# Optimization experiments

Measured on AMD Instinct MI355X. Metric: run time of the kernel, lower is better.

The kernel has to match this reference:

```python
import jax, jax.numpy as jnp
import numpy as np

D_MODEL = 1024
D_STATE = 16
D_CONV = 4
EXPAND = 2
D_INNER = D_MODEL * EXPAND


def setup_inputs() -> dict:
    key = jax.random.key(0)
    ks = jax.random.split(key, 8)
    B, L = 2, 2048
    x = jax.random.normal(ks[0], (B, L, D_MODEL), dtype=jnp.float32)
    # in_proj: Linear(d_model -> 2*d_inner), no bias
    W_in = jax.random.normal(ks[1], (D_MODEL, 2 * D_INNER), dtype=jnp.float32) / np.sqrt(D_MODEL)
    # depthwise conv1d: (d_inner, 1, d_conv) + bias
    conv_w = jax.random.normal(ks[2], (D_INNER, 1, D_CONV), dtype=jnp.float32) / np.sqrt(D_CONV)
    conv_b = jax.random.normal(ks[3], (D_INNER,), dtype=jnp.float32) * 0.01
    # x_proj: Linear(d_inner -> 2*d_state + 1), no bias
    W_x = jax.random.normal(ks[4], (D_INNER, 2 * D_STATE + 1), dtype=jnp.float32) / np.sqrt(D_INNER)
    # A_log ~ Uniform(-log(d_state), -1)
    A_log = jax.random.uniform(ks[5], (D_INNER, D_STATE), dtype=jnp.float32,
                               minval=-np.log(D_STATE), maxval=-1.0)
    D_param = jnp.ones((D_INNER,), dtype=jnp.float32)
    W_out = jax.random.normal(ks[6], (D_INNER, D_MODEL), dtype=jnp.float32) / np.sqrt(D_INNER)
    return {"x": x, "W_in": W_in, "conv_w": conv_w, "conv_b": conv_b,
            "W_x": W_x, "A_log": A_log, "D_param": D_param, "W_out": W_out}


def _selective_scan(x, delta, A, Bm, Cm):
    # x:(B,L,D), delta:(B,L), A:(D,N), Bm/Cm:(B,L,N)
    Bsz, L, Dd = x.shape
    N = A.shape[1]
    h0 = jnp.zeros((Bsz, Dd, N), dtype=x.dtype)

    def step(h, inp):
        dt, Bt, Ct, xt = inp  # (B,), wait dt:(B,), Bt:(B,N), Ct:(B,N), xt:(B,D)
        A_bar = jnp.exp(dt[:, None, None] * A)          # (B,D,N)
        dB = (dt[:, None] * Bt)[:, None, :]             # (B,1,N)
        h = A_bar * h + dB * xt[:, :, None]             # (B,D,N)
        y = jnp.einsum('bn,bdn->bd', Ct, h)             # (B,D)
        return h, y

    xs = (jnp.swapaxes(delta, 0, 1), jnp.swapaxes(Bm, 0, 1),
          jnp.swapaxes(Cm, 0, 1), jnp.swapaxes(x, 0, 1))
    _, ys = jax.lax.scan(step, h0, xs)                  # ys: (L,B,D)
    return jnp.swapaxes(ys, 0, 1)


def reference(x, W_in, conv_w, conv_b, W_x, A_log, D_param, W_out):
    B, L, _ = x.shape
    xr = x @ W_in                                       # (B,L,2*Di)
    x_inner, res = jnp.split(xr, 2, axis=-1)
    # causal depthwise conv: left-pad d_conv-1, valid conv == torch slice [:L]
    xc = jnp.swapaxes(x_inner, 1, 2)                    # (B,Di,L)
    xc = jax.lax.conv_general_dilated(
        xc, conv_w, window_strides=(1,), padding=[(D_CONV - 1, 0)],
        dimension_numbers=('NCH', 'OIH', 'NCH'), feature_group_count=D_INNER)
    xc = xc + conv_b[None, :, None]
    xc = jnp.swapaxes(xc, 1, 2)                         # (B,L,Di)
    xc = jax.nn.silu(xc)
    ssm_params = xc @ W_x                               # (B,L,1+2N)
    delta = jax.nn.softplus(ssm_params[..., 0])         # (B,L)
    Bm = ssm_params[..., 1:1 + D_STATE]                 # (B,L,N)
    Cm = ssm_params[..., 1 + D_STATE:]                  # (B,L,N)
    A = -jnp.exp(A_log)                                 # (Di,N)
    y = _selective_scan(xc, delta, A, Bm, Cm)           # (B,L,Di)
    y = y + xc * D_param[None, None, :]
    y = y * jax.nn.silu(res)
    return y @ W_out                                    # (B,L,d_model)
```

## Files before the change

### kernel.cpp

```cpp
#include <hip/hip_runtime.h>

#define L_SEQ 2048
#define NB    2
#define DMOD  1024
#define DIN   2048
#define NST   16
#define NROWS (NB*L_SEQ)
#define CL    32
#define NC    (L_SEQ/CL)

typedef unsigned short u16;
typedef _Float16 half8 __attribute__((ext_vector_type(8)));
typedef float f32x4 __attribute__((ext_vector_type(4)));
typedef short short8 __attribute__((ext_vector_type(8)));

__device__ __forceinline__ float siluf(float v){ return v / (1.f + __expf(-v)); }
__device__ __forceinline__ u16 f2h_bits(float v){ _Float16 h = (_Float16)v; return __builtin_bit_cast(u16, h); }
__device__ __forceinline__ float h2f(u16 v){ return (float)__builtin_bit_cast(_Float16, v); }
__device__ __forceinline__ float fexp2(float x){
#if __has_builtin(__builtin_amdgcn_exp2f)
    return __builtin_amdgcn_exp2f(x);
#else
    return __expf(x * 0.69314718056f);
#endif
}

__global__ __launch_bounds__(256)
void f32_to_f16(const float* __restrict__ in, u16* __restrict__ out, int n4)
{
    int i = blockIdx.x * 256 + threadIdx.x;
    if (i >= n4) return;
    float4 v = ((const float4*)in)[i];
    ushort4 o;
    o.x = f2h_bits(v.x); o.y = f2h_bits(v.y); o.z = f2h_bits(v.z); o.w = f2h_bits(v.w);
    *(ushort4*)&out[(size_t)i * 4] = o;
}

__global__ __launch_bounds__(256)
void transpose_to_f16(const float* __restrict__ in, u16* __restrict__ outT, int R, int C)
{
    __shared__ float s[64][65];
    int r0 = blockIdx.y * 64, c0 = blockIdx.x * 64;
    int tc = threadIdx.x & 63, ty = threadIdx.x >> 6;
    #pragma unroll
    for (int j = 0; j < 16; j++) {
        int r = ty + j * 4;
        s[r][tc] = in[(size_t)(r0 + r) * C + c0 + tc];
    }
    __syncthreads();
    #pragma unroll
    for (int j = 0; j < 16; j++) {
        int nn = ty + j * 4;
        outT[(size_t)(c0 + nn) * R + r0 + tc] = f2h_bits(s[tc][nn]);
    }
}

template<int EPI>
__global__ __launch_bounds__(256)
void gemm_mfma(const u16* __restrict__ A, const u16* __restrict__ Bt,
               void* __restrict__ C0v, void* __restrict__ C1v,
               int M, int N, int K)
{
    __shared__ __align__(16) u16 As[128 * 64];
    __shared__ __align__(16) u16 Bs[128 * 64];
    const int tid  = threadIdx.x;
    const int lane = tid & 63;
    const int wid  = tid >> 6;
    const int wm   = wid >> 1, wn = wid & 1;
    const int bm = blockIdx.y * 128, bn = blockIdx.x * 128;

    const int srow  = tid >> 3;
    const int sunit = tid & 7;
    const u16* Ag = A  + (size_t)bm * K;
    const u16* Bg = Bt + (size_t)bn * K;

    f32x4 acc[4][4];
    #pragma unroll
    for (int i = 0; i < 4; i++)
        #pragma unroll
        for (int j = 0; j < 4; j++)
            acc[i][j] = (f32x4){0.f, 0.f, 0.f, 0.f};

    short8 ra[4], rb[4];
    #pragma unroll
    for (int j = 0; j < 4; j++) {
        int row = j * 32 + srow;
        ra[j] = *(const short8*)&Ag[(size_t)row * K + sunit * 8];
        rb[j] = *(const short8*)&Bg[(size_t)row * K + sunit * 8];
    }

    for (int k0 = 0; k0 < K; k0 += 64) {
        __syncthreads();
        #pragma unroll
        for (int j = 0; j < 4; j++) {
            int row  = j * 32 + srow;
            int slot = sunit ^ (row & 7);
            *(short8*)&As[row * 64 + slot * 8] = ra[j];
            *(short8*)&Bs[row * 64 + slot * 8] = rb[j];
        }
        __syncthreads();
        if (k0 + 64 < K) {
            #pragma unroll
            for (int j = 0; j < 4; j++) {
                int row = j * 32 + srow;
                ra[j] = *(const short8*)&Ag[(size_t)row * K + k0 + 64 + sunit * 8];
                rb[j] = *(const short8*)&Bg[(size_t)row * K + k0 + 64 + sunit * 8];
            }
        }
        #pragma unroll
        for (int kk = 0; kk < 2; kk++) {
            half8 af[4], bf[4];
            #pragma unroll
            for (int mi = 0; mi < 4; mi++) {
                int row  = wm * 64 + mi * 16 + (lane & 15);
                int slot = (kk * 4 + (lane >> 4)) ^ (row & 7);
                af[mi] = *(const half8*)&As[row * 64 + slot * 8];
            }
            #pragma unroll
            for (int ni = 0; ni < 4; ni++) {
                int row  = wn * 64 + ni * 16 + (lane & 15);
                int slot = (kk * 4 + (lane >> 4)) ^ (row & 7);
                bf[ni] = *(const half8*)&Bs[row * 64 + slot * 8];
            }
            #pragma unroll
            for (int mi = 0; mi < 4; mi++)
                #pragma unroll
                for (int ni = 0; ni < 4; ni++)
                    acc[mi][ni] = __builtin_amdgcn_mfma_f32_16x16x32_f16(af[mi], bf[ni], acc[mi][ni], 0, 0, 0);
        }
    }

    const int cr = (lane >> 4) * 4;
    const int cc = lane & 15;
    #pragma unroll
    for (int mi = 0; mi < 4; mi++) {
        #pragma unroll
        for (int ni = 0; ni < 4; ni++) {
            #pragma unroll
            for (int q = 0; q < 4; q++) {
                int row = bm + wm * 64 + mi * 16 + cr + q;
                int col = bn + wn * 64 + ni * 16 + cc;
                float v = acc[mi][ni][q];
                if (EPI == 0) {
                    ((float*)C0v)[(size_t)row * N + col] = v;
                } else {
                    int half = N >> 1;
                    if (col < half) ((u16*)C0v)[(size_t)row * half + col] = f2h_bits(v);
                    else            ((u16*)C1v)[(size_t)row * half + col - half] = f2h_bits(siluf(v));
                }
            }
        }
    }
}

__global__ __launch_bounds__(256)
void conv_silu16(const u16* __restrict__ xin16, const float* __restrict__ cw,
                 const float* __restrict__ cb, u16* __restrict__ xc16)
{
    int idx = blockIdx.x * 256 + threadIdx.x;
    int d8 = idx & 255;
    int t  = (idx >> 8) & (L_SEQ - 1);
    int b  = idx >> 19;
    int d  = d8 << 3;
    const float4* cw4 = (const float4*)cw;
    float4 w[8];
    #pragma unroll
    for (int j = 0; j < 8; j++) w[j] = cw4[d + j];
    float acc[8];
    {
        float4 b0 = *(const float4*)&cb[d];
        float4 b1 = *(const float4*)&cb[d + 4];
        acc[0]=b0.x; acc[1]=b0.y; acc[2]=b0.z; acc[3]=b0.w;
        acc[4]=b1.x; acc[5]=b1.y; acc[6]=b1.z; acc[7]=b1.w;
    }
    #pragma unroll
    for (int k = 0; k < 4; k++) {
        int tt = t + k - 3;
        if (tt >= 0) {
            short8 v = *(const short8*)&xin16[((size_t)(b * L_SEQ + tt)) * DIN + d];
            #pragma unroll
            for (int j = 0; j < 8; j++)
                acc[j] = fmaf(h2f((u16)v[j]), (&w[j].x)[k], acc[j]);
        }
    }
    short8 o;
    #pragma unroll
    for (int j = 0; j < 8; j++) o[j] = (short)f2h_bits(siluf(acc[j]));
    *(short8*)&xc16[(size_t)idx * 8] = o;
}

__global__ __launch_bounds__(256)
void transpose_wx16(const float* __restrict__ Wx, u16* __restrict__ WxT16)
{
    int idx = blockIdx.x * 256 + threadIdx.x;
    int n = idx >> 11, k = idx & 2047;
    float v = (n < 33) ? Wx[k * 33 + n] : 0.f;
    WxT16[idx] = f2h_bits(v);
}

__global__ __launch_bounds__(256)
void gemm2_mfma(const u16* __restrict__ A, const u16* __restrict__ Bt, float* __restrict__ pb)
{
    __shared__ __align__(16) u16 As[64 * 64];
    __shared__ __align__(16) u16 Bs[48 * 64];
    const int tid = threadIdx.x, lane = tid & 63, w = tid >> 6;
    const int bm = blockIdx.x * 64;
    const int kz = blockIdx.y;
    const int arow = tid >> 2;
    const int au   = (tid & 3) << 1;
    f32x4 acc[3];
    acc[0] = acc[1] = acc[2] = (f32x4){0.f, 0.f, 0.f, 0.f};

    for (int it = 0; it < 4; ++it) {
        const int k0 = kz * 256 + it * 64;
        short8 ra0 = *(const short8*)&A[(size_t)(bm + arow) * DIN + k0 + au * 8];
        short8 ra1 = *(const short8*)&A[(size_t)(bm + arow) * DIN + k0 + (au + 1) * 8];
        short8 rb0, rb1;
        if (tid < 192) {
            rb0 = *(const short8*)&Bt[(size_t)arow * DIN + k0 + au * 8];
            rb1 = *(const short8*)&Bt[(size_t)arow * DIN + k0 + (au + 1) * 8];
        }
        __syncthreads();
        {
            int s0 = au ^ (arow & 7), s1 = (au + 1) ^ (arow & 7);
            *(short8*)&As[arow * 64 + s0 * 8] = ra0;
            *(short8*)&As[arow * 64 + s1 * 8] = ra1;
            if (tid < 192) {
                *(short8*)&Bs[arow * 64 + s0 * 8] = rb0;
                *(short8*)&Bs[arow * 64 + s1 * 8] = rb1;
            }
        }
        __syncthreads();
        #pragma unroll
        for (int kk = 0; kk < 2; kk++) {
            int r = w * 16 + (lane & 15);
            int sl = (kk * 4 + (lane >> 4)) ^ (r & 7);
            half8 af = *(const half8*)&As[r * 64 + sl * 8];
            #pragma unroll
            for (int ni = 0; ni < 3; ni++) {
                int br = ni * 16 + (lane & 15);
                int bsl = (kk * 4 + (lane >> 4)) ^ (br & 7);
                half8 bf = *(const half8*)&Bs[br * 64 + bsl * 8];
                acc[ni] = __builtin_amdgcn_mfma_f32_16x16x32_f16(af, bf, acc[ni], 0, 0, 0);
            }
        }
    }
    #pragma unroll
    for (int ni = 0; ni < 3; ni++) {
        #pragma unroll
        for (int q = 0; q < 4; q++) {
            int row = bm + w * 16 + (lane >> 4) * 4 + q;
            int col = ni * 16 + (lane & 15);
            pb[((size_t)kz * NROWS + row) * 48 + col] = acc[ni][q];
        }
    }
}

__global__ __launch_bounds__(256)
void gemm2_reduce(const float* __restrict__ pb, float* __restrict__ delta,
                  float* __restrict__ Bm, float* __restrict__ Cm)
{
    int idx = blockIdx.x * 256 + threadIdx.x;
    int row = idx / 48, col = idx - row * 48;
    float s = 0.f;
    #pragma unroll
    for (int kz = 0; kz < 8; kz++) s += pb[(size_t)kz * NROWS * 48 + idx];
    if (col == 0)       delta[row] = fmaxf(s, 0.f) + log1pf(__expf(-fabsf(s)));
    else if (col < 17)  Bm[row * NST + col - 1]  = s;
    else if (col < 33)  Cm[row * NST + col - 17] = s;
}

__global__ __launch_bounds__(256)
void scan_part1_reg(const u16* __restrict__ xc16, const float* __restrict__ delta,
                    const float* __restrict__ Bm, const float* __restrict__ A_log,
                    float* __restrict__ h_loc, float* __restrict__ Pc)
{
    const int b = blockIdx.z, c = blockIdx.y;
    const int d = blockIdx.x * 256 + threadIdx.x;
    float ka[16];
    {
        const float4* Av = (const float4*)(A_log + (size_t)d * 16);
        #pragma unroll
        for (int q = 0; q < 4; q++) {
            float4 a = Av[q];
            ka[q*4+0] = -__expf(a.x) * 1.44269504f;
            ka[q*4+1] = -__expf(a.y) * 1.44269504f;
            ka[q*4+2] = -__expf(a.z) * 1.44269504f;
            ka[q*4+3] = -__expf(a.w) * 1.44269504f;
        }
    }
    float h[16];
    #pragma unroll
    for (int n = 0; n < 16; n++) h[n] = 0.f;
    float S = 0.f;
    const int rowbase = b * L_SEQ + c * CL;
    #pragma unroll 2
    for (int t = 0; t < CL; ++t) {
        const int rowg = rowbase + t;
        const float dt = delta[rowg];
        const float4* Bv = (const float4*)(Bm + (size_t)rowg * 16);
        float4 b0 = Bv[0], b1 = Bv[1], b2 = Bv[2], b3 = Bv[3];
        float bb[16] = {b0.x,b0.y,b0.z,b0.w, b1.x,b1.y,b1.z,b1.w,
                        b2.x,b2.y,b2.z,b2.w, b3.x,b3.y,b3.z,b3.w};
        const float xt = h2f(xc16[(size_t)rowg * DIN + d]);
        const float dtx = dt * xt;
        S += dt;
        #pragma unroll
        for (int n = 0; n < 16; n++) {
            float a = fexp2(dt * ka[n]);
            h[n] = fmaf(a, h[n], bb[n] * dtx);
        }
    }
    float* hp = h_loc + (((size_t)(b * NC + c) * DIN) + d) * 16;
    float* pp = Pc    + (((size_t)(b * NC + c) * DIN) + d) * 16;
    #pragma unroll
    for (int q = 0; q < 4; q++) {
        *(float4*)&hp[q*4] = (float4){h[q*4+0], h[q*4+1], h[q*4+2], h[q*4+3]};
        *(float4*)&pp[q*4] = (float4){fexp2(S*ka[q*4+0]), fexp2(S*ka[q*4+1]),
                                      fexp2(S*ka[q*4+2]), fexp2(S*ka[q*4+3])};
    }
}

__global__ __launch_bounds__(256)
void scan_carry(const float* __restrict__ h_loc, const float* __restrict__ Pc,
                float* __restrict__ H_in)
{
    int gid = blockIdx.x * 256 + threadIdx.x;
    int b = gid >> 15, r = gid & 32767;
    float H = 0.f;
    for (int c = 0; c < NC; ++c) {
        size_t idx = ((size_t)(b * NC + c) << 15) + r;
        H_in[idx] = H;
        H = fmaf(Pc[idx], H, h_loc[idx]);
    }
}

__global__ __launch_bounds__(256)
void scan_part3_reg(const u16* __restrict__ xc16, const float* __restrict__ delta,
                    const float* __restrict__ Bm, const float* __restrict__ Cm,
                    const float* __restrict__ A_log, const float* __restrict__ Dp,
                    const u16* __restrict__ res16, const float* __restrict__ H_in,
                    u16* __restrict__ yh)
{
    const int b = blockIdx.z, c = blockIdx.y;
    const int d = blockIdx.x * 256 + threadIdx.x;
    float ka[16];
    {
        const float4* Av = (const float4*)(A_log + (size_t)d * 16);
        #pragma unroll
        for (int q = 0; q < 4; q++) {
            float4 a = Av[q];
            ka[q*4+0] = -__expf(a.x) * 1.44269504f;
            ka[q*4+1] = -__expf(a.y) * 1.44269504f;
            ka[q*4+2] = -__expf(a.z) * 1.44269504f;
            ka[q*4+3] = -__expf(a.w) * 1.44269504f;
        }
    }
    float h[16];
    {
        const float4* Hv = (const float4*)(H_in + (((size_t)(b * NC + c) * DIN) + d) * 16);
        #pragma unroll
        for (int q = 0; q < 4; q++) {
            float4 v = Hv[q];
            h[q*4+0]=v.x; h[q*4+1]=v.y; h[q*4+2]=v.z; h[q*4+3]=v.w;
        }
    }
    const float Dpd = Dp[d];
    const int rowbase = b * L_SEQ + c * CL;
    #pragma unroll 2
    for (int t = 0; t < CL; ++t) {
        const int rowg = rowbase + t;
        const float dt = delta[rowg];
        const float4* Bv = (const float4*)(Bm + (size_t)rowg * 16);
        const float4* Cv = (const float4*)(Cm + (size_t)rowg * 16);
        float4 b0 = Bv[0], b1 = Bv[1], b2 = Bv[2], b3 = Bv[3];
        float4 c0 = Cv[0], c1 = Cv[1], c2 = Cv[2], c3 = Cv[3];
        float bb[16] = {b0.x,b0.y,b0.z,b0.w, b1.x,b1.y,b1.z,b1.w,
                        b2.x,b2.y,b2.z,b2.w, b3.x,b3.y,b3.z,b3.w};
        float cc[16] = {c0.x,c0.y,c0.z,c0.w, c1.x,c1.y,c1.z,c1.w,
                        c2.x,c2.y,c2.z,c2.w, c3.x,c3.y,c3.z,c3.w};
        const float xt = h2f(xc16[(size_t)rowg * DIN + d]);
        const float rt = h2f(res16[(size_t)rowg * DIN + d]);
        const float dtx = dt * xt;
        float y = 0.f;
        #pragma unroll
        for (int n = 0; n < 16; n++) {
            float a = fexp2(dt * ka[n]);
            h[n] = fmaf(a, h[n], bb[n] * dtx);
            y = fmaf(cc[n], h[n], y);
        }
        y = (y + xt * Dpd) * rt;
        yh[(size_t)rowg * DIN + d] = f2h_bits(y);
    }
}

extern "C" void kernel_launch(void* const* d_in, const int* in_sizes, int n_in,
                              void* d_out, int out_size, void* d_ws, size_t ws_size,
                              hipStream_t stream)
{
    const float* x     = (const float*)d_in[0];
    const float* W_in  = (const float*)d_in[1];
    const float* cw    = (const float*)d_in[2];
    const float* cb    = (const float*)d_in[3];
    const float* Wx    = (const float*)d_in[4];
    const float* A_log = (const float*)d_in[5];
    const float* Dp    = (const float*)d_in[6];
    const float* W_out = (const float*)d_in[7];
    float* out = (float*)d_out;
    float* ws  = (float*)d_ws;

    u16*   xin16 = (u16*)(ws);
    u16*   y16   = (u16*)(ws);
    u16*   res16 = (u16*)(ws + 4194304);
    u16*   xc16  = (u16*)(ws + 8388608);
    u16*   x16   = (u16*)(ws + 12582912);
    u16*   Bt3   = (u16*)(ws + 12582912);
    u16*   Bt1   = (u16*)(ws + 14680064);
    float* pb    = ws + 14680064;
    u16*   WxT16 = (u16*)(ws + 16252928);
    float* delta = ws + 16777216;
    float* Bm    = ws + 16781312;
    float* Cm    = ws + 16846848;
    float* h_loc = ws + 16912384;
    float* Pc    = ws + 21106688;
    float* H_in  = ws + 25300992;

    dim3 blk(256);

    f32_to_f16<<<dim3(NROWS * DMOD / 4 / 256), blk, 0, stream>>>(x, x16, NROWS * DMOD / 4);
    transpose_to_f16<<<dim3(4096 / 64, 1024 / 64), blk, 0, stream>>>(W_in, Bt1, DMOD, 2 * DIN);
    gemm_mfma<1><<<dim3(32, 32), blk, 0, stream>>>(x16, Bt1, xin16, res16, NROWS, 2 * DIN, DMOD);
    conv_silu16<<<dim3(NB * L_SEQ * (DIN / 8) / 256), blk, 0, stream>>>(xin16, cw, cb, xc16);
    transpose_wx16<<<dim3(48 * DIN / 256), blk, 0, stream>>>(Wx, WxT16);
    gemm2_mfma<<<dim3(NROWS / 64, 8), blk, 0, stream>>>(xc16, WxT16, pb);
    gemm2_reduce<<<dim3(NROWS * 48 / 256), blk, 0, stream>>>(pb, delta, Bm, Cm);
    scan_part1_reg<<<dim3(DIN / 256, NC, NB), blk, 0, stream>>>(xc16, delta, Bm, A_log, h_loc, Pc);
    scan_carry<<<dim3(NB * DIN * NST / 256), blk, 0, stream>>>(h_loc, Pc, H_in);
    scan_part3_reg<<<dim3(DIN / 256, NC, NB), blk, 0, stream>>>(xc16, delta, Bm, Cm, A_log, Dp, res16, H_in, y16);
    transpose_to_f16<<<dim3(1024 / 64, 2048 / 64), blk, 0, stream>>>(W_out, Bt3, DIN, DMOD);
    gemm_mfma<0><<<dim3(1024 / 128, NROWS / 128), blk, 0, stream>>>(y16, Bt3, out, nullptr, NROWS, DMOD, DIN);
}
```

Baseline: 209.0 us.

## Load GEMM tiles straight into LDS with global_load_lds and lengthen scan chunks

The MFMA GEMM drops register-staged prefetch and the swizzled LDS layout. It now issues direct global-to-LDS 16-byte loads with a K-step of 32, which cuts register pressure and copy instructions. In exchange it loses the overlap of the next tile's load with compute, and the unswizzled LDS reads may hit bank conflicts. The scan chunk length doubles from 32 to 64, halving the chunk count and the carry and state buffers, so the workspace layout is repacked.

```diff
diff --git a/kernel.cpp b/kernel.cpp
--- a/kernel.cpp
+++ b/kernel.cpp
@@ -6,7 +6,7 @@
 #define DIN   2048
 #define NST   16
 #define NROWS (NB*L_SEQ)
-#define CL    32
+#define CL    64
 #define NC    (L_SEQ/CL)
 
 typedef unsigned short u16;
@@ -25,6 +25,14 @@
 #endif
 }
 
+__device__ __forceinline__ void gload16(const u16* g, u16* l)
+{
+    __builtin_amdgcn_global_load_lds(
+        (const __attribute__((address_space(1))) void*)g,
+        (__attribute__((address_space(3))) void*)l,
+        16, 0, 0);
+}
+
 __global__ __launch_bounds__(256)
 void f32_to_f16(const float* __restrict__ in, u16* __restrict__ out, int n4)
 {
@@ -61,18 +69,18 @@
                void* __restrict__ C0v, void* __restrict__ C1v,
                int M, int N, int K)
 {
-    __shared__ __align__(16) u16 As[128 * 64];
-    __shared__ __align__(16) u16 Bs[128 * 64];
+    __shared__ __align__(16) u16 As[128 * 32];
+    __shared__ __align__(16) u16 Bs[128 * 32];
     const int tid  = threadIdx.x;
     const int lane = tid & 63;
     const int wid  = tid >> 6;
     const int wm   = wid >> 1, wn = wid & 1;
     const int bm = blockIdx.y * 128, bn = blockIdx.x * 128;
 
-    const int srow  = tid >> 3;
-    const int sunit = tid & 7;
-    const u16* Ag = A  + (size_t)bm * K;
-    const u16* Bg = Bt + (size_t)bn * K;
+    const int sunit = lane & 3;
+    const int srow  = lane >> 2;
+    const u16* Ag = A  + (size_t)bm * K + sunit * 8;
+    const u16* Bg = Bt + (size_t)bn * K + sunit * 8;
 
     f32x4 acc[4][4];
     #pragma unroll
@@ -81,53 +89,32 @@
         for (int j = 0; j < 4; j++)
             acc[i][j] = (f32x4){0.f, 0.f, 0.f, 0.f};
 
-    short8 ra[4], rb[4];
-    #pragma unroll
-    for (int j = 0; j < 4; j++) {
-        int row = j * 32 + srow;
-        ra[j] = *(const short8*)&Ag[(size_t)row * K + sunit * 8];
-        rb[j] = *(const short8*)&Bg[(size_t)row * K + sunit * 8];
-    }
-
-    for (int k0 = 0; k0 < K; k0 += 64) {
+    for (int k0 = 0; k0 < K; k0 += 32) {
         __syncthreads();
         #pragma unroll
-        for (int j = 0; j < 4; j++) {
-            int row  = j * 32 + srow;
-            int slot = sunit ^ (row & 7);
-            *(short8*)&As[row * 64 + slot * 8] = ra[j];
-            *(short8*)&Bs[row * 64 + slot * 8] = rb[j];
+        for (int j = 0; j < 2; j++) {
+            int row = wid * 32 + j * 16 + srow;
+            gload16(Ag + (size_t)row * K + k0, &As[(wid * 2 + j) * 512]);
+            gload16(Bg + (size_t)row * K + k0, &Bs[(wid * 2 + j) * 512]);
         }
         __syncthreads();
-        if (k0 + 64 < K) {
+
+        half8 af[4], bf[4];
+        #pragma unroll
+        for (int mi = 0; mi < 4; mi++) {
+            int row = wm * 64 + mi * 16 + (lane & 15);
+            af[mi] = *(const half8*)&As[row * 32 + (lane >> 4) * 8];
+        }
+        #pragma unroll
+        for (int ni = 0; ni < 4; ni++) {
+            int row = wn * 64 + ni * 16 + (lane & 15);
+            bf[ni] = *(const half8*)&Bs[row * 32 + (lane >> 4) * 8];
+        }
+        #pragma unroll
+        for (int mi = 0; mi < 4; mi++)
             #pragma unroll
-            for (int j = 0; j < 4; j++) {
-                int row = j * 32 + srow;
-                ra[j] = *(const short8*)&Ag[(size_t)row * K + k0 + 64 + sunit * 8];
-                rb[j] = *(const short8*)&Bg[(size_t)row * K + k0 + 64 + sunit * 8];
-            }
-        }
-        #pragma unroll
-        for (int kk = 0; kk < 2; kk++) {
-            half8 af[4], bf[4];
-            #pragma unroll
-            for (int mi = 0; mi < 4; mi++) {
-                int row  = wm * 64 + mi * 16 + (lane & 15);
-                int slot = (kk * 4 + (lane >> 4)) ^ (row & 7);
-                af[mi] = *(const half8*)&As[row * 64 + slot * 8];
-            }
-            #pragma unroll
-            for (int ni = 0; ni < 4; ni++) {
-                int row  = wn * 64 + ni * 16 + (lane & 15);
-                int slot = (kk * 4 + (lane >> 4)) ^ (row & 7);
-                bf[ni] = *(const half8*)&Bs[row * 64 + slot * 8];
-            }
-            #pragma unroll
-            for (int mi = 0; mi < 4; mi++)
-                #pragma unroll
-                for (int ni = 0; ni < 4; ni++)
-                    acc[mi][ni] = __builtin_amdgcn_mfma_f32_16x16x32_f16(af[mi], bf[ni], acc[mi][ni], 0, 0, 0);
-        }
+            for (int ni = 0; ni < 4; ni++)
+                acc[mi][ni] = __builtin_amdgcn_mfma_f32_16x16x32_f16(af[mi], bf[ni], acc[mi][ni], 0, 0, 0);
     }
 
     const int cr = (lane >> 4) * 4;
@@ -417,13 +404,13 @@
     u16*   Bt3   = (u16*)(ws + 12582912);
     u16*   Bt1   = (u16*)(ws + 14680064);
     float* pb    = ws + 14680064;
-    u16*   WxT16 = (u16*)(ws + 16252928);
-    float* delta = ws + 16777216;
-    float* Bm    = ws + 16781312;
-    float* Cm    = ws + 16846848;
-    float* h_loc = ws + 16912384;
-    float* Pc    = ws + 21106688;
-    float* H_in  = ws + 25300992;
+    u16*   WxT16 = (u16*)(ws + 16777216);
+    float* delta = ws + 16826368;
+    float* Bm    = ws + 16830464;
+    float* Cm    = ws + 16896000;
+    float* h_loc = ws + 16961536;
+    float* Pc    = ws + 19058688;
+    float* H_in  = ws + 21155840;
 
     dim3 blk(256);
 
```

After: 244.0 us. 1.17x slower.
